# Kernel optimization log

Measured on AMD Instinct MI355X. Metric: run time of the kernel, lower is better.

The kernel has to match this reference:

```python
import jax, jax.numpy as jnp
import numpy as np

DT = 0.01
KKT_REG = 1e-3  # small Tikhonov regularization for the all-active KKT proxy


def _forward(x, v, cld, dist, mu, cor, Minv):
    bs, n, d = x.shape  # d == 2
    nc = cld.shape[1]
    nd = n * d
    i, j = cld[..., 0], cld[..., 1]
    # contact point positions (n_p == 1 so object == point)
    p1 = jnp.take_along_axis(x, i[..., None], axis=1)  # [bs, nc, 2]
    p2 = jnp.take_along_axis(x, j[..., None], axis=1)
    diff = p2 - p1
    e_n = diff / jnp.linalg.norm(diff, axis=-1, keepdims=True)  # contact normal
    e_t = jnp.stack([-e_n[..., 1], e_n[..., 0]], axis=-1)       # tangent (d=2)
    # contact Jacobian [bs, nc, 2(normal/tangent), n, d]; c_tilde == 1 for n_p=1
    bi = jnp.arange(bs)[:, None]
    ci = jnp.arange(nc)[None, :]
    Jac = jnp.zeros((bs, nc, 2, n, d), x.dtype)
    Jac = Jac.at[bi, ci, 0, i].set(-e_n)
    Jac = Jac.at[bi, ci, 0, j].set(e_n)
    Jac = Jac.at[bi, ci, 1, i].set(-e_t)
    Jac = Jac.at[bi, ci, 1, j].set(e_t)
    J_cn = Jac[:, :, 0].reshape(bs, nc, nd)          # normal rows
    Jt = Jac[:, :, 1].reshape(bs, nc, nd)            # tangent rows
    # interleaved +/- tangent rows: J_ct[0::2]=Jt, J_ct[1::2]=-Jt
    J_ct = jnp.stack([Jt, -Jt], axis=2).reshape(bs, 2 * nc, nd)
    M = jnp.linalg.inv(Minv)
    pM = jnp.kron(M, jnp.eye(d, dtype=x.dtype))      # populated_M[i::d, i::d] = M
    E = jnp.kron(jnp.eye(nc, dtype=x.dtype), jnp.ones((2, 1), x.dtype))  # [2nc, nc]
    vflat = v.reshape(bs, nd)
    Mv = vflat @ pM.T
    Jcnv = jnp.einsum('bcj,bj->bc', J_cn, vflat)
    v_star0 = -dist / DT / 8.0
    h = jnp.concatenate([jnp.minimum(-v_star0, cor * Jcnv),
                         jnp.zeros((bs, 3 * nc), x.dtype)], axis=1)  # [bs, 4nc]
    G = jnp.concatenate([J_cn, J_ct, jnp.zeros((bs, nc, nd), x.dtype)], axis=1)
    m = 4 * nc
    F = jnp.zeros((bs, m, m), x.dtype)
    F = F.at[:, 3 * nc:, :nc].set(jax.vmap(jnp.diag)(mu))
    F = F.at[:, nc:3 * nc, 3 * nc:].set(E)
    F = F.at[:, 3 * nc:, nc:3 * nc].set(-E.T)
    # lcp_solver(pM, Mv, G, h, [], [], -F) replaced by the all-active KKT solve:
    #   [pM  G^T] [z]   [-Mv]
    #   [G   -F ] [l] = [-h ]
    K = jnp.zeros((bs, nd + m, nd + m), x.dtype)
    K = K.at[:, :nd, :nd].set(pM)
    K = K.at[:, :nd, nd:].set(jnp.swapaxes(G, 1, 2))
    K = K.at[:, nd:, :nd].set(G)
    K = K.at[:, nd:, nd:].set(-F)
    K = K + KKT_REG * jnp.eye(nd + m, dtype=x.dtype)
    rhs = jnp.concatenate([-Mv, -h], axis=1)
    sol = jnp.linalg.solve(K, rhs[..., None])[..., 0]
    v_plus = -sol[:, :nd]
    # torch.stack([x, new_v], 1).reshape(bs, -1)
    return jnp.concatenate([x.reshape(bs, nd), v_plus], axis=1)


def setup_inputs() -> dict:
    key = jax.random.key(0)
    ks = jax.random.split(key, 8)
    bs, n, nc = 1024, 64, 32
    x = jax.random.normal(ks[0], (bs, n, 2), jnp.float32)
    v = jax.random.normal(ks[1], (bs, n, 2), jnp.float32)
    i = jax.random.randint(ks[2], (bs, nc), 0, n // 2)
    j = jax.random.randint(ks[3], (bs, nc), n // 2, n)
    cld_ij_ids = jnp.stack([i, j], axis=-1).astype(jnp.int32)
    dist_ij = -0.1 * jax.random.uniform(ks[4], (bs, nc), jnp.float32)
    mu = jax.random.uniform(ks[5], (bs, nc), jnp.float32)
    cor = jax.random.uniform(ks[6], (bs, nc), jnp.float32)
    A = jax.random.normal(ks[7], (n, n), jnp.float32)
    Minv = A @ A.T / n + jnp.eye(n, dtype=jnp.float32)  # SPD inverse mass matrix
    return {"x": x, "v": v, "cld_ij_ids": cld_ij_ids, "dist_ij": dist_ij,
            "mu": mu, "cor": cor, "Minv": Minv}


def reference(x, v, cld_ij_ids, dist_ij, mu, cor, Minv):
    return _forward(x, v, cld_ij_ids, dist_ij, mu, cor, Minv)
```

## Files before the change

### kernel.cpp

```cpp
#include <hip/hip_runtime.h>
#include <math.h>


#define NBODY 64
#define NC    32
#define ND    128
#define EPS   1e-3f
#define WPAD  65

__device__ __forceinline__ float readlane_f(float x, int lane) {
  return __int_as_float(__builtin_amdgcn_readlane(__float_as_int(x), lane));
}

__device__ __forceinline__ float rcp_fast(float x) {
  float r;
  asm("v_rcp_f32 %0, %1" : "=v"(r) : "v"(x));
  return r;
}

__global__ __launch_bounds__(64) void precompute_W(
    const float* __restrict__ Minv, float* __restrict__ Wg) {
  const int lane = threadIdx.x;
  const int col = blockIdx.x;

  float Mr[NBODY];
  const float4* mv = (const float4*)(Minv + lane * NBODY);
#pragma unroll
  for (int e4 = 0; e4 < 16; ++e4) {
    float4 t = mv[e4];
    Mr[4 * e4] = t.x; Mr[4 * e4 + 1] = t.y;
    Mr[4 * e4 + 2] = t.z; Mr[4 * e4 + 3] = t.w;
  }

  const float dlt = (lane == col) ? 1.0f : 0.0f;
  float s = dlt;
#pragma unroll
  for (int t = 0; t < 6; ++t) {
    float a0 = 0.f, a1 = 0.f, a2 = 0.f, a3 = 0.f;
#pragma unroll
    for (int e = 0; e < NBODY; e += 4) {
      a0 = fmaf(Mr[e],     readlane_f(s, e),     a0);
      a1 = fmaf(Mr[e + 1], readlane_f(s, e + 1), a1);
      a2 = fmaf(Mr[e + 2], readlane_f(s, e + 2), a2);
      a3 = fmaf(Mr[e + 3], readlane_f(s, e + 3), a3);
    }
    s = dlt - EPS * ((a0 + a1) + (a2 + a3));
  }
  float a0 = 0.f, a1 = 0.f, a2 = 0.f, a3 = 0.f;
#pragma unroll
  for (int e = 0; e < NBODY; e += 4) {
    a0 = fmaf(Mr[e],     readlane_f(s, e),     a0);
    a1 = fmaf(Mr[e + 1], readlane_f(s, e + 1), a1);
    a2 = fmaf(Mr[e + 2], readlane_f(s, e + 2), a2);
    a3 = fmaf(Mr[e + 3], readlane_f(s, e + 3), a3);
  }
  Wg[lane * NBODY + col] = (a0 + a1) + (a2 + a3);
}

__global__ __launch_bounds__(256, 4) void solve_batch(
    const float* __restrict__ x, const float* __restrict__ v,
    const int* __restrict__ cld, const float* __restrict__ dist,
    const float* __restrict__ cor, const float* __restrict__ Wg,
    float* __restrict__ out) {
  __shared__ float Wl[NBODY * WPAD];
  __shared__ float vw[ND], qw[ND], yw[ND];
  __shared__ float4 mrow[2][64];
  __shared__ float dv[64];

  const int tid  = threadIdx.x;
  const int w    = tid >> 6;
  const int lane = tid & 63;
  const int b    = blockIdx.x;

  for (int idx = tid; idx < NBODY * NBODY; idx += 256)
    Wl[(idx >> 6) * WPAD + (idx & 63)] = Wg[idx];

  const float* xb = x + b * ND;
  const float* vb = v + b * ND;

  const int half = w & 1;
  const int t = lane + 64 * half;
  if (w < 2) vw[t] = vb[t];

  const int rc = lane & 31;
  const int myi = cld[b * 2 * NC + 2 * rc];
  const int myj = cld[b * 2 * NC + 2 * rc + 1];
  float dx = xb[2 * myj]     - xb[2 * myi];
  float dy = xb[2 * myj + 1] - xb[2 * myi + 1];
  float il = 1.0f / sqrtf(dx * dx + dy * dy);
  float enx = dx * il, eny = dy * il;
  float wx = (lane < 32) ? enx : -eny;
  float wy = (lane < 32) ? eny : enx;

  __syncthreads();

  const int kc = lane & 1;
  const int a  = t >> 1;
  const float* Wa = Wl + a * WPAD;
  if (w < 2) {
    float s = 0.f;
    for (int e = 0; e < NBODY; ++e) s = fmaf(Wa[e], vw[2 * e + kc], s);
    qw[t] = vw[t] - EPS * s;
  }

  float rowq[16];
  const float* Wi = Wl + myi * WPAD;
  const float* Wj = Wl + myj * WPAD;
#pragma unroll
  for (int q = 0; q < 16; ++q) {
    int c = 16 * (q >> 2) + 4 * w + (q & 3);
    int ic = __builtin_amdgcn_readlane(myi, c);
    int jc = __builtin_amdgcn_readlane(myj, c);
    float wcx = readlane_f(wx, c);
    float wcy = readlane_f(wy, c);
    float kap = (Wi[ic] - Wi[jc]) - (Wj[ic] - Wj[jc]);
    float aa = (wx * wcx + wy * wcy) * kap;
    aa = (c == lane) ? aa - ((lane < 32) ? EPS : 0.5f * EPS) : aa;
    rowq[q] = aa;
  }

  __syncthreads();

  float rhs;
  {
    float qdx = qw[2 * myj]     - qw[2 * myi];
    float qdy = qw[2 * myj + 1] - qw[2 * myi + 1];
    float h = 0.0f;
    if (lane < 32) {
      float vdx = vw[2 * myj]     - vw[2 * myi];
      float vdy = vw[2 * myj + 1] - vw[2 * myi + 1];
      float jcnv = enx * vdx + eny * vdy;
      h = fminf(dist[b * NC + rc] * 12.5f, cor[b * NC + rc] * jcnv);
    }
    rhs = h - (wx * qdx + wy * qdy);
  }

#pragma unroll
  for (int g = 0; g < 16; ++g) {
    const int om = g & 3;
    const int gc = g >> 2;
    float m0, m1, m2, m3;
    if (w == om) {
      const int base = 4 * gc;
      {
        const int k = 4 * g;
        float r = rcp_fast(readlane_f(rowq[base], k));
        if (lane == k) dv[k] = r;
        m0 = (lane == k) ? 0.f : rowq[base] * r;
        rowq[base+1] = fmaf(-m0, readlane_f(rowq[base+1], k), rowq[base+1]);
        rowq[base+2] = fmaf(-m0, readlane_f(rowq[base+2], k), rowq[base+2]);
        rowq[base+3] = fmaf(-m0, readlane_f(rowq[base+3], k), rowq[base+3]);
      }
      {
        const int k = 4 * g + 1;
        float r = rcp_fast(readlane_f(rowq[base+1], k));
        if (lane == k) dv[k] = r;
        m1 = (lane == k) ? 0.f : rowq[base+1] * r;
        rowq[base+2] = fmaf(-m1, readlane_f(rowq[base+2], k), rowq[base+2]);
        rowq[base+3] = fmaf(-m1, readlane_f(rowq[base+3], k), rowq[base+3]);
      }
      {
        const int k = 4 * g + 2;
        float r = rcp_fast(readlane_f(rowq[base+2], k));
        if (lane == k) dv[k] = r;
        m2 = (lane == k) ? 0.f : rowq[base+2] * r;
        rowq[base+3] = fmaf(-m2, readlane_f(rowq[base+3], k), rowq[base+3]);
      }
      {
        const int k = 4 * g + 3;
        float r = rcp_fast(readlane_f(rowq[base+3], k));
        if (lane == k) dv[k] = r;
        m3 = (lane == k) ? 0.f : rowq[base+3] * r;
      }
      mrow[g & 1][lane] = make_float4(m0, m1, m2, m3);
    }
    __syncthreads();
    if (w != om) {
      float4 mv = mrow[g & 1][lane];
      m0 = mv.x; m1 = mv.y; m2 = mv.z; m3 = mv.w;
    }
    rhs = fmaf(-m0, readlane_f(rhs, 4 * g),     rhs);
    rhs = fmaf(-m1, readlane_f(rhs, 4 * g + 1), rhs);
    rhs = fmaf(-m2, readlane_f(rhs, 4 * g + 2), rhs);
    rhs = fmaf(-m3, readlane_f(rhs, 4 * g + 3), rhs);
#pragma unroll
    for (int cl = 0; cl < 4; ++cl) {
      if (cl < gc) continue;
      if ((cl > gc) || (w > om)) {
#pragma unroll
        for (int within = 0; within < 4; ++within) {
          const int q = 4 * cl + within;
          rowq[q] = fmaf(-m0, readlane_f(rowq[q], 4 * g),     rowq[q]);
          rowq[q] = fmaf(-m1, readlane_f(rowq[q], 4 * g + 1), rowq[q]);
          rowq[q] = fmaf(-m2, readlane_f(rowq[q], 4 * g + 2), rowq[q]);
          rowq[q] = fmaf(-m3, readlane_f(rowq[q], 4 * g + 3), rowq[q]);
        }
      }
    }
  }

  if (w >= 2) return;

  float myx = rhs * dv[lane];

  {
    float y = 0.f;
#pragma unroll
    for (int c = 0; c < NC; ++c) {
      float ex = readlane_f(wx, c),      ey = readlane_f(wy, c);
      float tx = readlane_f(wx, c + 32), ty = readlane_f(wy, c + 32);
      float lam = readlane_f(myx, c);
      float del = readlane_f(myx, c + 32);
      float wk = (kc ? ey : ex) * lam + (kc ? ty : tx) * del;
      if (w == 0) {
        int ic = __builtin_amdgcn_readlane(myi, c);
        y -= (ic == a) ? wk : 0.0f;
      } else {
        int jc = __builtin_amdgcn_readlane(myj, c);
        y += (jc == a) ? wk : 0.0f;
      }
    }
    yw[t] = y;
  }
  __syncthreads();

  {
    float s = 0.f;
    for (int e = 0; e < NBODY; ++e) s = fmaf(Wa[e], yw[2 * e + kc], s);
    float* ob = out + b * 256;
    ob[t]       = xb[t];
    ob[128 + t] = qw[t] + s;
  }
}

extern "C" void kernel_launch(void* const* d_in, const int* in_sizes, int n_in,
                              void* d_out, int out_size, void* d_ws, size_t ws_size,
                              hipStream_t stream) {
  const float* x    = (const float*)d_in[0];
  const float* v    = (const float*)d_in[1];
  const int*   cld  = (const int*)  d_in[2];
  const float* dist = (const float*)d_in[3];
  const float* cor  = (const float*)d_in[5];
  const float* Minv = (const float*)d_in[6];
  float* out = (float*)d_out;

  const int bs = in_sizes[0] / ND;
  float* W = (float*)d_ws;

  precompute_W<<<NBODY, 64, 0, stream>>>(Minv, W);
  solve_batch<<<bs, 256, 0, stream>>>(x, v, cld, dist, cor, W, out);
}
```

Baseline: 93.18 us.

## Widen Gauss-Jordan panel to eight columns and fold rhs setup into loop

Switches the in-register elimination from sixteen panels of four columns to eight panels of eight, which halves the number of block-wide barriers and shared-memory multiplier exchanges. The rhs setup no longer has its own barrier; it runs after the first loop barrier, and the h term is computed earlier. q is also kept in a register for the final output. In exchange, each serial panel step is longer on the owning wave while the other waves wait, and the extra multipliers and unrolled loops raise register pressure.

```diff
diff --git a/kernel.cpp b/kernel.cpp
--- a/kernel.cpp
+++ b/kernel.cpp
@@ -64,7 +64,8 @@
     float* __restrict__ out) {
   __shared__ float Wl[NBODY * WPAD];
   __shared__ float vw[ND], qw[ND], yw[ND];
-  __shared__ float4 mrow[2][64];
+  __shared__ float4 mrowA[2][64];
+  __shared__ float4 mrowB[2][64];
   __shared__ float dv[64];
 
   const int tid  = threadIdx.x;
@@ -97,10 +98,20 @@
   const int kc = lane & 1;
   const int a  = t >> 1;
   const float* Wa = Wl + a * WPAD;
+  float qreg = 0.f;
   if (w < 2) {
     float s = 0.f;
     for (int e = 0; e < NBODY; ++e) s = fmaf(Wa[e], vw[2 * e + kc], s);
-    qw[t] = vw[t] - EPS * s;
+    qreg = vw[t] - EPS * s;
+    qw[t] = qreg;
+  }
+
+  float hterm = 0.0f;
+  if (lane < 32) {
+    float vdx = vw[2 * myj]     - vw[2 * myi];
+    float vdy = vw[2 * myj + 1] - vw[2 * myi + 1];
+    float jcnv = enx * vdx + eny * vdy;
+    hterm = fminf(dist[b * NC + rc] * 12.5f, cor[b * NC + rc] * jcnv);
   }
 
   float rowq[16];
@@ -108,7 +119,7 @@
   const float* Wj = Wl + myj * WPAD;
 #pragma unroll
   for (int q = 0; q < 16; ++q) {
-    int c = 16 * (q >> 2) + 4 * w + (q & 3);
+    int c = 32 * (q >> 3) + 8 * w + (q & 7);
     int ic = __builtin_amdgcn_readlane(myi, c);
     int jc = __builtin_amdgcn_readlane(myj, c);
     float wcx = readlane_f(wx, c);
@@ -119,81 +130,53 @@
     rowq[q] = aa;
   }
 
-  __syncthreads();
-
-  float rhs;
-  {
-    float qdx = qw[2 * myj]     - qw[2 * myi];
-    float qdy = qw[2 * myj + 1] - qw[2 * myi + 1];
-    float h = 0.0f;
-    if (lane < 32) {
-      float vdx = vw[2 * myj]     - vw[2 * myi];
-      float vdy = vw[2 * myj + 1] - vw[2 * myi + 1];
-      float jcnv = enx * vdx + eny * vdy;
-      h = fminf(dist[b * NC + rc] * 12.5f, cor[b * NC + rc] * jcnv);
-    }
-    rhs = h - (wx * qdx + wy * qdy);
-  }
-
-#pragma unroll
-  for (int g = 0; g < 16; ++g) {
+  float rhs = 0.0f;
+#pragma unroll
+  for (int g = 0; g < 8; ++g) {
     const int om = g & 3;
     const int gc = g >> 2;
-    float m0, m1, m2, m3;
+    float m[8];
     if (w == om) {
-      const int base = 4 * gc;
-      {
-        const int k = 4 * g;
-        float r = rcp_fast(readlane_f(rowq[base], k));
+      const int base = 8 * gc;
+#pragma unroll
+      for (int s = 0; s < 8; ++s) {
+        const int k = 8 * g + s;
+        float r = rcp_fast(readlane_f(rowq[base + s], k));
         if (lane == k) dv[k] = r;
-        m0 = (lane == k) ? 0.f : rowq[base] * r;
-        rowq[base+1] = fmaf(-m0, readlane_f(rowq[base+1], k), rowq[base+1]);
-        rowq[base+2] = fmaf(-m0, readlane_f(rowq[base+2], k), rowq[base+2]);
-        rowq[base+3] = fmaf(-m0, readlane_f(rowq[base+3], k), rowq[base+3]);
+        m[s] = (lane == k) ? 0.f : rowq[base + s] * r;
+#pragma unroll
+        for (int u = s + 1; u < 8; ++u)
+          rowq[base + u] = fmaf(-m[s], readlane_f(rowq[base + u], k),
+                                rowq[base + u]);
       }
-      {
-        const int k = 4 * g + 1;
-        float r = rcp_fast(readlane_f(rowq[base+1], k));
-        if (lane == k) dv[k] = r;
-        m1 = (lane == k) ? 0.f : rowq[base+1] * r;
-        rowq[base+2] = fmaf(-m1, readlane_f(rowq[base+2], k), rowq[base+2]);
-        rowq[base+3] = fmaf(-m1, readlane_f(rowq[base+3], k), rowq[base+3]);
-      }
-      {
-        const int k = 4 * g + 2;
-        float r = rcp_fast(readlane_f(rowq[base+2], k));
-        if (lane == k) dv[k] = r;
-        m2 = (lane == k) ? 0.f : rowq[base+2] * r;
-        rowq[base+3] = fmaf(-m2, readlane_f(rowq[base+3], k), rowq[base+3]);
-      }
-      {
-        const int k = 4 * g + 3;
-        float r = rcp_fast(readlane_f(rowq[base+3], k));
-        if (lane == k) dv[k] = r;
-        m3 = (lane == k) ? 0.f : rowq[base+3] * r;
-      }
-      mrow[g & 1][lane] = make_float4(m0, m1, m2, m3);
+      mrowA[g & 1][lane] = make_float4(m[0], m[1], m[2], m[3]);
+      mrowB[g & 1][lane] = make_float4(m[4], m[5], m[6], m[7]);
     }
     __syncthreads();
+    if (g == 0) {
+      float qdx = qw[2 * myj]     - qw[2 * myi];
+      float qdy = qw[2 * myj + 1] - qw[2 * myi + 1];
+      rhs = hterm - (wx * qdx + wy * qdy);
+    }
     if (w != om) {
-      float4 mv = mrow[g & 1][lane];
-      m0 = mv.x; m1 = mv.y; m2 = mv.z; m3 = mv.w;
-    }
-    rhs = fmaf(-m0, readlane_f(rhs, 4 * g),     rhs);
-    rhs = fmaf(-m1, readlane_f(rhs, 4 * g + 1), rhs);
-    rhs = fmaf(-m2, readlane_f(rhs, 4 * g + 2), rhs);
-    rhs = fmaf(-m3, readlane_f(rhs, 4 * g + 3), rhs);
-#pragma unroll
-    for (int cl = 0; cl < 4; ++cl) {
+      float4 ma = mrowA[g & 1][lane];
+      float4 mb = mrowB[g & 1][lane];
+      m[0] = ma.x; m[1] = ma.y; m[2] = ma.z; m[3] = ma.w;
+      m[4] = mb.x; m[5] = mb.y; m[6] = mb.z; m[7] = mb.w;
+    }
+#pragma unroll
+    for (int s = 0; s < 8; ++s)
+      rhs = fmaf(-m[s], readlane_f(rhs, 8 * g + s), rhs);
+#pragma unroll
+    for (int cl = 0; cl < 2; ++cl) {
       if (cl < gc) continue;
       if ((cl > gc) || (w > om)) {
 #pragma unroll
-        for (int within = 0; within < 4; ++within) {
-          const int q = 4 * cl + within;
-          rowq[q] = fmaf(-m0, readlane_f(rowq[q], 4 * g),     rowq[q]);
-          rowq[q] = fmaf(-m1, readlane_f(rowq[q], 4 * g + 1), rowq[q]);
-          rowq[q] = fmaf(-m2, readlane_f(rowq[q], 4 * g + 2), rowq[q]);
-          rowq[q] = fmaf(-m3, readlane_f(rowq[q], 4 * g + 3), rowq[q]);
+        for (int within = 0; within < 8; ++within) {
+          const int q = 8 * cl + within;
+#pragma unroll
+          for (int s = 0; s < 8; ++s)
+            rowq[q] = fmaf(-m[s], readlane_f(rowq[q], 8 * g + s), rowq[q]);
         }
       }
     }
@@ -229,7 +212,7 @@
     for (int e = 0; e < NBODY; ++e) s = fmaf(Wa[e], yw[2 * e + kc], s);
     float* ob = out + b * 256;
     ob[t]       = xb[t];
-    ob[128 + t] = qw[t] + s;
+    ob[128 + t] = qreg + s;
   }
 }
 
```

Measured after the change: 92.51 us. About the same (-0.7%).
